# Kernel optimization log

Measured on AMD Instinct MI355X. Metric: run time of the kernel, lower is better.

The kernel has to match this reference:

```python
import jax, jax.numpy as jnp
import numpy as np

B, T, D, H = 2, 2048, 1024, 16  # batch, seq, n_embed, n_head


def setup_inputs() -> dict:
    key = jax.random.key(0)
    ks = jax.random.split(key, 5)
    scale = 1.0 / np.sqrt(D)
    return {
        "x": jax.random.normal(ks[0], (B, T, D), dtype=jnp.float32),
        "Wq": jax.random.normal(ks[1], (D, D), dtype=jnp.float32) * scale,
        "Wk": jax.random.normal(ks[2], (D, D), dtype=jnp.float32) * scale,
        "Wv": jax.random.normal(ks[3], (D, D), dtype=jnp.float32) * scale,
        "Wo": jax.random.normal(ks[4], (D, D), dtype=jnp.float32) * scale,
    }


def reference(x, Wq, Wk, Wv, Wo):
    b, t, d = x.shape
    hd = d // H  # head_dim
    # projections -> [B, H, T, hd]
    q = (x @ Wq).reshape(b, t, H, hd).transpose(0, 2, 1, 3)
    k = (x @ Wk).reshape(b, t, H, hd).transpose(0, 2, 1, 3)
    v = (x @ Wv).reshape(b, t, H, hd).transpose(0, 2, 1, 3)
    # scaled scores [B, H, T, T] with causal mask
    e = jnp.einsum("bhqd,bhkd->bhqk", q, k) * (1.0 / np.sqrt(hd))
    causal = jnp.tril(jnp.ones((t, t), dtype=bool))
    e = jnp.where(causal[None, None], e, jnp.finfo(e.dtype).min)
    alpha = jax.nn.softmax(e, axis=-1)
    # attention output -> [B, T, D]
    attn = jnp.einsum("bhqk,bhkd->bhqd", alpha, v)
    attn = attn.transpose(0, 2, 1, 3).reshape(b, t, d)
    return attn @ Wo
```

## Files before the change

### kernel.cpp

```cpp
#include <hip/hip_runtime.h>
#include <hip/hip_bf16.h>
#include <math.h>


#define Bsz  2
#define Tseq 2048
#define Dm   1024
#define NH   16
#define HD   64

typedef short bf16x8 __attribute__((ext_vector_type(8)));
typedef float floatx4 __attribute__((ext_vector_type(4)));

__device__ __forceinline__ unsigned short f2bf(float f) {
    __hip_bfloat16 h = __float2bfloat16(f);
    return *reinterpret_cast<unsigned short*>(&h);
}

__device__ __forceinline__ unsigned short f2bf_fast(float f) {
    unsigned int u = __builtin_bit_cast(unsigned int, f);
    return (unsigned short)((u + 0x8000u) >> 16);
}

__device__ __forceinline__ void lds16(unsigned short* lds, const unsigned short* g) {
    __builtin_amdgcn_global_load_lds(
        (const __attribute__((address_space(1))) void*)g,
        (__attribute__((address_space(3))) void*)lds, 16, 0, 0);
}

__global__ __launch_bounds__(256) void prep(const float* __restrict__ x,
                                            const float* __restrict__ W0,
                                            const float* __restrict__ W1,
                                            const float* __restrict__ W2,
                                            const float* __restrict__ W3,
                                            unsigned short* __restrict__ xb,
                                            unsigned short* __restrict__ T0,
                                            unsigned short* __restrict__ T1,
                                            unsigned short* __restrict__ T2,
                                            unsigned short* __restrict__ T3) {
    __shared__ float t[64][65];
    const int z = blockIdx.z;
    if (z >= 4) {
        const int bi = (z - 4) * 256 + blockIdx.y * 16 + blockIdx.x;
        const size_t i = (size_t)bi * 256 + threadIdx.x;
        const float4 v = ((const float4*)x)[i];
        ushort4 o;
        o.x = f2bf(v.x); o.y = f2bf(v.y); o.z = f2bf(v.z); o.w = f2bf(v.w);
        ((ushort4*)xb)[i] = o;
        return;
    }
    const float* W = (z == 0) ? W0 : (z == 1) ? W1 : (z == 2) ? W2 : W3;
    unsigned short* T = (z == 0) ? T0 : (z == 1) ? T1 : (z == 2) ? T2 : T3;
    const int k0 = blockIdx.y * 64, n0 = blockIdx.x * 64;
    const int row = threadIdx.x >> 6, col = threadIdx.x & 63;
#pragma unroll
    for (int p = 0; p < 16; ++p)
        t[p * 4 + row][col] = W[(size_t)(k0 + p * 4 + row) * Dm + n0 + col];
    __syncthreads();
#pragma unroll
    for (int p = 0; p < 16; ++p)
        T[(size_t)(n0 + p * 4 + row) * Dm + k0 + col] = f2bf(t[col][p * 4 + row]);
}

__device__ __forceinline__ void gemm128_mainloop(const unsigned short* __restrict__ A,
                                                 const unsigned short* __restrict__ Bt,
                                                 int K, int m0, int n0,
                                                 unsigned short* As, unsigned short* Bs,
                                                 floatx4 acc[4][4]) {
    const int tid = threadIdx.x;
    const int lane = tid & 63, wave = tid >> 6;
    const int l15 = lane & 15, quad = lane >> 4;
    const int wm = (wave >> 1) * 64, wn = (wave & 1) * 64;

    for (int k0 = 0; k0 < K; k0 += 32) {
        __syncthreads();
#pragma unroll
        for (int c = 0; c < 2; ++c) {
            const int idx = c * 256 + tid;
            const int row = idx >> 2, kc = (idx & 3) * 8;
            lds16(&As[row * 32 + kc], A + (size_t)(m0 + row) * K + k0 + kc);
            lds16(&Bs[row * 32 + kc], Bt + (size_t)(n0 + row) * K + k0 + kc);
        }
        __syncthreads();
        bf16x8 af[4], bf[4];
#pragma unroll
        for (int i = 0; i < 4; ++i)
            af[i] = *(const bf16x8*)&As[(wm + i * 16 + l15) * 32 + quad * 8];
#pragma unroll
        for (int j = 0; j < 4; ++j)
            bf[j] = *(const bf16x8*)&Bs[(wn + j * 16 + l15) * 32 + quad * 8];
#pragma unroll
        for (int i = 0; i < 4; ++i)
#pragma unroll
            for (int j = 0; j < 4; ++j)
                acc[i][j] = __builtin_amdgcn_mfma_f32_16x16x32_bf16(af[i], bf[j], acc[i][j], 0, 0, 0);
    }
}

__global__ __launch_bounds__(256) void gemm_qkv(const unsigned short* __restrict__ xb,
                                                const unsigned short* __restrict__ Wqt,
                                                const unsigned short* __restrict__ Wkt,
                                                const unsigned short* __restrict__ Wvt,
                                                unsigned short* __restrict__ Qb,
                                                unsigned short* __restrict__ Kb,
                                                unsigned short* __restrict__ VbT) {
    __shared__ unsigned short As[128 * 32];
    __shared__ unsigned short Bs[128 * 32];
    const int z = blockIdx.z;
    const unsigned short* Bt = (z == 0) ? Wqt : (z == 1) ? Wkt : Wvt;
    const float scale = (z == 0) ? (0.125f * 1.4426950408889634f) : 1.0f;
    const int m0 = blockIdx.y * 128, n0 = blockIdx.x * 128;

    floatx4 acc[4][4];
#pragma unroll
    for (int i = 0; i < 4; ++i)
#pragma unroll
        for (int j = 0; j < 4; ++j) acc[i][j] = (floatx4){0.f, 0.f, 0.f, 0.f};

    gemm128_mainloop(xb, Bt, Dm, m0, n0, As, Bs, acc);

    const int lane = threadIdx.x & 63, wave = threadIdx.x >> 6;
    const int l15 = lane & 15, quad = lane >> 4;
    const int wm = (wave >> 1) * 64, wn = (wave & 1) * 64;

    if (z == 2) {
#pragma unroll
        for (int i = 0; i < 4; ++i)
#pragma unroll
            for (int j = 0; j < 4; ++j) {
                const int col = n0 + wn + j * 16 + l15;
                const int hh = col >> 6, dd = col & 63;
                const int tok = m0 + wm + i * 16 + quad * 4;
                const int bb = tok >> 11, tl = tok & (Tseq - 1);
                ushort4 o;
                o.x = f2bf(acc[i][j][0]); o.y = f2bf(acc[i][j][1]);
                o.z = f2bf(acc[i][j][2]); o.w = f2bf(acc[i][j][3]);
                *(ushort4*)&VbT[((size_t)((bb * NH + hh) * HD + dd)) * Tseq + tl] = o;
            }
        return;
    }
    unsigned short* C = (z == 0) ? Qb : Kb;
#pragma unroll
    for (int i = 0; i < 4; ++i)
#pragma unroll
        for (int j = 0; j < 4; ++j)
#pragma unroll
            for (int r = 0; r < 4; ++r) {
                const int row = m0 + wm + i * 16 + quad * 4 + r;
                const int col = n0 + wn + j * 16 + l15;
                C[(size_t)row * Dm + col] = f2bf(acc[i][j][r] * scale);
            }
}

__global__ __launch_bounds__(256) void gemm_out(const unsigned short* __restrict__ Yb,
                                                const unsigned short* __restrict__ Wot,
                                                float* __restrict__ out) {
    __shared__ unsigned short As[64 * 32];
    __shared__ unsigned short Bs[64 * 32];
    const int m0 = blockIdx.y * 64, n0 = blockIdx.x * 64;
    const int tid = threadIdx.x;
    const int lane = tid & 63, wave = tid >> 6;
    const int l15 = lane & 15, quad = lane >> 4;
    const int wm = (wave >> 1) * 32, wn = (wave & 1) * 32;

    floatx4 acc[2][2];
#pragma unroll
    for (int i = 0; i < 2; ++i)
#pragma unroll
        for (int j = 0; j < 2; ++j) acc[i][j] = (floatx4){0.f, 0.f, 0.f, 0.f};

    const int srow = tid >> 2, kc = (tid & 3) * 8;

    for (int k0 = 0; k0 < Dm; k0 += 32) {
        __syncthreads();
        lds16(&As[srow * 32 + kc], Yb + (size_t)(m0 + srow) * Dm + k0 + kc);
        lds16(&Bs[srow * 32 + kc], Wot + (size_t)(n0 + srow) * Dm + k0 + kc);
        __syncthreads();
        bf16x8 af[2], bf[2];
#pragma unroll
        for (int i = 0; i < 2; ++i)
            af[i] = *(const bf16x8*)&As[(wm + i * 16 + l15) * 32 + quad * 8];
#pragma unroll
        for (int j = 0; j < 2; ++j)
            bf[j] = *(const bf16x8*)&Bs[(wn + j * 16 + l15) * 32 + quad * 8];
#pragma unroll
        for (int i = 0; i < 2; ++i)
#pragma unroll
            for (int j = 0; j < 2; ++j)
                acc[i][j] = __builtin_amdgcn_mfma_f32_16x16x32_bf16(af[i], bf[j], acc[i][j], 0, 0, 0);
    }

#pragma unroll
    for (int i = 0; i < 2; ++i)
#pragma unroll
        for (int j = 0; j < 2; ++j)
#pragma unroll
            for (int r = 0; r < 4; ++r) {
                const int row = m0 + wm + i * 16 + quad * 4 + r;
                const int col = n0 + wn + j * 16 + l15;
                out[(size_t)row * Dm + col] = acc[i][j][r];
            }
}

__global__ __launch_bounds__(256) void attn_mfma(const unsigned short* __restrict__ Qb,
                                                 const unsigned short* __restrict__ Kb,
                                                 const unsigned short* __restrict__ VbT,
                                                 unsigned short* __restrict__ Yb) {
    const int bh = blockIdx.x;
    const int b = bh >> 4;
    const int h = bh & 15;
    const int qt = 31 - blockIdx.y;
    const int tid = threadIdx.x;
    const int wave = tid >> 6;
    const int lane = tid & 63;
    const int l15 = lane & 15;
    const int quad = lane >> 4;

    __shared__ unsigned short Ks0[2][64][32];
    __shared__ unsigned short Ks1[2][64][32];
    __shared__ unsigned short Vt0[2][64][32];
    __shared__ unsigned short Vt1[2][64][32];
    __shared__ unsigned short Ps[4][16][72];

    const size_t tok0 = (size_t)b * Tseq;
    const int colh = h * HD;
    const unsigned short* vbase = VbT + (size_t)bh * HD * Tseq;

    const int qrow = qt * 64 + wave * 16;

    const unsigned short* qptr = Qb + (tok0 + qrow + l15) * Dm + colh + quad * 8;
    const bf16x8 qf0 = *(const bf16x8*)(qptr);
    const bf16x8 qf1 = *(const bf16x8*)(qptr + 32);

    float l_lane = 0.f;
    floatx4 o_acc[4];
#pragma unroll
    for (int t = 0; t < 4; ++t) o_acc[t] = (floatx4){0.f, 0.f, 0.f, 0.f};

    const int srow = tid >> 2;
    const int sc8 = (tid & 3) * 8;
    const int ssw = ((tid & 3) ^ ((srow >> 1) & 3)) * 8;
    const int qsw = (quad ^ ((l15 >> 1) & 3)) * 8;

    const int niter = (qt + 2) >> 1;
    for (int it = 0; it < niter; ++it) {
        const int k0 = it * 128;
        __syncthreads();
#pragma unroll
        for (int s = 0; s < 2; ++s) {
            const unsigned short* krow = Kb + (tok0 + k0 + s * 64 + srow) * Dm + colh;
            const unsigned short* vrow = vbase + (size_t)srow * Tseq + k0 + s * 64;
            lds16(&Ks0[s][srow][sc8], krow + ssw);
            lds16(&Ks1[s][srow][sc8], krow + 32 + ssw);
            lds16(&Vt0[s][srow][sc8], vrow + ssw);
            lds16(&Vt1[s][srow][sc8], vrow + 32 + ssw);
        }
        __syncthreads();

#pragma unroll
        for (int s = 0; s < 2; ++s) {
            const int k0s = k0 + s * 64;
            if (k0s > qrow + 15) continue;

            floatx4 sf[4];
#pragma unroll
            for (int t = 0; t < 4; ++t) {
                floatx4 c = (floatx4){0.f, 0.f, 0.f, 0.f};
                const bf16x8 kb0 = *(const bf16x8*)&Ks0[s][t * 16 + l15][qsw];
                const bf16x8 kb1 = *(const bf16x8*)&Ks1[s][t * 16 + l15][qsw];
                c = __builtin_amdgcn_mfma_f32_16x16x32_bf16(kb0, qf0, c, 0, 0, 0);
                c = __builtin_amdgcn_mfma_f32_16x16x32_bf16(kb1, qf1, c, 0, 0, 0);
                sf[t] = c;
            }

            if (k0s + 63 > qrow) {
                const int ql = qrow + l15;
#pragma unroll
                for (int t = 0; t < 4; ++t)
#pragma unroll
                    for (int r = 0; r < 4; ++r) {
                        const int kl = k0s + t * 16 + quad * 4 + r;
                        if (kl > ql) sf[t][r] = -1.0e30f;
                    }
            }

#pragma unroll
            for (int t = 0; t < 4; ++t) {
                float p0 = __builtin_amdgcn_exp2f(sf[t][0]);
                float p1 = __builtin_amdgcn_exp2f(sf[t][1]);
                float p2 = __builtin_amdgcn_exp2f(sf[t][2]);
                float p3 = __builtin_amdgcn_exp2f(sf[t][3]);
                l_lane += (p0 + p1) + (p2 + p3);
                ushort4 o;
                o.x = f2bf_fast(p0); o.y = f2bf_fast(p1);
                o.z = f2bf_fast(p2); o.w = f2bf_fast(p3);
                *(ushort4*)&Ps[wave][l15][t * 16 + quad * 4] = o;
            }

            const bf16x8 pa0 = *(const bf16x8*)&Ps[wave][l15][quad * 8];
            const bf16x8 pa1 = *(const bf16x8*)&Ps[wave][l15][32 + quad * 8];
#pragma unroll
            for (int t = 0; t < 4; ++t) {
                const bf16x8 vb0 = *(const bf16x8*)&Vt0[s][t * 16 + l15][qsw];
                const bf16x8 vb1 = *(const bf16x8*)&Vt1[s][t * 16 + l15][qsw];
                o_acc[t] = __builtin_amdgcn_mfma_f32_16x16x32_bf16(pa0, vb0, o_acc[t], 0, 0, 0);
                o_acc[t] = __builtin_amdgcn_mfma_f32_16x16x32_bf16(pa1, vb1, o_acc[t], 0, 0, 0);
            }
        }
    }

    l_lane += __shfl_xor(l_lane, 16);
    l_lane += __shfl_xor(l_lane, 32);
    const float inv_q = 1.0f / l_lane;
    float inv_r[4];
#pragma unroll
    for (int r = 0; r < 4; ++r)
        inv_r[r] = __shfl(inv_q, (lane & 48) | (quad * 4 + r));
#pragma unroll
    for (int t = 0; t < 4; ++t)
#pragma unroll
        for (int r = 0; r < 4; ++r) {
            const int q = qrow + quad * 4 + r;
            Yb[(tok0 + q) * Dm + colh + t * 16 + l15] = f2bf(o_acc[t][r] * inv_r[r]);
        }
}

extern "C" void kernel_launch(void* const* d_in, const int* in_sizes, int n_in,
                              void* d_out, int out_size, void* d_ws, size_t ws_size,
                              hipStream_t stream) {
    const float* x  = (const float*)d_in[0];
    const float* Wq = (const float*)d_in[1];
    const float* Wk = (const float*)d_in[2];
    const float* Wv = (const float*)d_in[3];
    const float* Wo = (const float*)d_in[4];
    float* out = (float*)d_out;

    const int M = Bsz * Tseq;
    char* ws = (char*)d_ws;
    unsigned short* xb  = (unsigned short*)(ws);
    unsigned short* Wqt = (unsigned short*)(ws + (((size_t)8)  << 20));
    unsigned short* Wkt = (unsigned short*)(ws + (((size_t)10) << 20));
    unsigned short* Wvt = (unsigned short*)(ws + (((size_t)12) << 20));
    unsigned short* Wot = (unsigned short*)(ws + (((size_t)14) << 20));
    unsigned short* Qb  = (unsigned short*)(ws + (((size_t)16) << 20));
    unsigned short* Kb  = (unsigned short*)(ws + (((size_t)24) << 20));
    unsigned short* VbT = (unsigned short*)(ws + (((size_t)32) << 20));
    unsigned short* Yb  = (unsigned short*)(ws + (((size_t)40) << 20));

    dim3 blk(256);
    hipLaunchKernelGGL(prep, dim3(16, 16, 20), blk, 0, stream,
                       x, Wq, Wk, Wv, Wo, xb, Wqt, Wkt, Wvt, Wot);

    hipLaunchKernelGGL(gemm_qkv, dim3(Dm / 128, M / 128, 3), blk, 0, stream,
                       xb, Wqt, Wkt, Wvt, Qb, Kb, VbT);

    hipLaunchKernelGGL(attn_mfma, dim3(Bsz * NH, 32), blk, 0, stream, Qb, Kb, VbT, Yb);

    hipLaunchKernelGGL(gemm_out, dim3(Dm / 64, M / 64), blk, 0, stream, Yb, Wot, out);
}
```

Before: 168.0 us.

## Double-buffer K/V tiles in attention kernel and raise MFMA wave priority

Adds a second LDS buffer for the K and V tiles, prefetched with async global-to-LDS loads. The next 128-key tile now loads while the current one is computed, with one vmcnt wait and barrier per iteration instead of two syncthreads around a blocking load. It also raises the wave priority (s_setprio) around the MFMA blocks. This doubles the LDS footprint of the attention kernel, which may lower occupancy.

```diff
diff --git a/kernel.cpp b/kernel.cpp
--- a/kernel.cpp
+++ b/kernel.cpp
@@ -216,10 +216,10 @@
     const int l15 = lane & 15;
     const int quad = lane >> 4;
 
-    __shared__ unsigned short Ks0[2][64][32];
-    __shared__ unsigned short Ks1[2][64][32];
-    __shared__ unsigned short Vt0[2][64][32];
-    __shared__ unsigned short Vt1[2][64][32];
+    __shared__ unsigned short Ks0[2][2][64][32];
+    __shared__ unsigned short Ks1[2][2][64][32];
+    __shared__ unsigned short Vt0[2][2][64][32];
+    __shared__ unsigned short Vt1[2][2][64][32];
     __shared__ unsigned short Ps[4][16][72];
 
     const size_t tok0 = (size_t)b * Tseq;
@@ -243,19 +243,41 @@
     const int qsw = (quad ^ ((l15 >> 1) & 3)) * 8;
 
     const int niter = (qt + 2) >> 1;
+
+    {
+        const unsigned short* krow0 = Kb + (tok0 + srow) * Dm + colh;
+        const unsigned short* krow1 = Kb + (tok0 + 64 + srow) * Dm + colh;
+        const unsigned short* vrow = vbase + (size_t)srow * Tseq;
+        lds16(&Ks0[0][0][srow][sc8], krow0 + ssw);
+        lds16(&Ks1[0][0][srow][sc8], krow0 + 32 + ssw);
+        lds16(&Vt0[0][0][srow][sc8], vrow + ssw);
+        lds16(&Vt1[0][0][srow][sc8], vrow + 32 + ssw);
+        lds16(&Ks0[0][1][srow][sc8], krow1 + ssw);
+        lds16(&Ks1[0][1][srow][sc8], krow1 + 32 + ssw);
+        lds16(&Vt0[0][1][srow][sc8], vrow + 64 + ssw);
+        lds16(&Vt1[0][1][srow][sc8], vrow + 64 + 32 + ssw);
+    }
+    asm volatile("s_waitcnt vmcnt(0)" ::: "memory");
+    __builtin_amdgcn_s_barrier();
+    __builtin_amdgcn_sched_barrier(0);
+
     for (int it = 0; it < niter; ++it) {
         const int k0 = it * 128;
-        __syncthreads();
-#pragma unroll
-        for (int s = 0; s < 2; ++s) {
-            const unsigned short* krow = Kb + (tok0 + k0 + s * 64 + srow) * Dm + colh;
-            const unsigned short* vrow = vbase + (size_t)srow * Tseq + k0 + s * 64;
-            lds16(&Ks0[s][srow][sc8], krow + ssw);
-            lds16(&Ks1[s][srow][sc8], krow + 32 + ssw);
-            lds16(&Vt0[s][srow][sc8], vrow + ssw);
-            lds16(&Vt1[s][srow][sc8], vrow + 32 + ssw);
+        const int bi = it & 1;
+
+        if (it + 1 < niter) {
+            const int kn = k0 + 128;
+#pragma unroll
+            for (int s = 0; s < 2; ++s) {
+                const unsigned short* krow = Kb + (tok0 + kn + s * 64 + srow) * Dm + colh;
+                const unsigned short* vrow = vbase + (size_t)srow * Tseq + kn + s * 64;
+                lds16(&Ks0[bi ^ 1][s][srow][sc8], krow + ssw);
+                lds16(&Ks1[bi ^ 1][s][srow][sc8], krow + 32 + ssw);
+                lds16(&Vt0[bi ^ 1][s][srow][sc8], vrow + ssw);
+                lds16(&Vt1[bi ^ 1][s][srow][sc8], vrow + 32 + ssw);
+            }
         }
-        __syncthreads();
+        __builtin_amdgcn_sched_barrier(0);
 
 #pragma unroll
         for (int s = 0; s < 2; ++s) {
@@ -263,15 +285,17 @@
             if (k0s > qrow + 15) continue;
 
             floatx4 sf[4];
+            __builtin_amdgcn_s_setprio(1);
 #pragma unroll
             for (int t = 0; t < 4; ++t) {
                 floatx4 c = (floatx4){0.f, 0.f, 0.f, 0.f};
-                const bf16x8 kb0 = *(const bf16x8*)&Ks0[s][t * 16 + l15][qsw];
-                const bf16x8 kb1 = *(const bf16x8*)&Ks1[s][t * 16 + l15][qsw];
+                const bf16x8 kb0 = *(const bf16x8*)&Ks0[bi][s][t * 16 + l15][qsw];
+                const bf16x8 kb1 = *(const bf16x8*)&Ks1[bi][s][t * 16 + l15][qsw];
                 c = __builtin_amdgcn_mfma_f32_16x16x32_bf16(kb0, qf0, c, 0, 0, 0);
                 c = __builtin_amdgcn_mfma_f32_16x16x32_bf16(kb1, qf1, c, 0, 0, 0);
                 sf[t] = c;
             }
+            __builtin_amdgcn_s_setprio(0);
 
             if (k0s + 63 > qrow) {
                 const int ql = qrow + l15;
@@ -299,14 +323,20 @@
 
             const bf16x8 pa0 = *(const bf16x8*)&Ps[wave][l15][quad * 8];
             const bf16x8 pa1 = *(const bf16x8*)&Ps[wave][l15][32 + quad * 8];
+            __builtin_amdgcn_s_setprio(1);
 #pragma unroll
             for (int t = 0; t < 4; ++t) {
-                const bf16x8 vb0 = *(const bf16x8*)&Vt0[s][t * 16 + l15][qsw];
-                const bf16x8 vb1 = *(const bf16x8*)&Vt1[s][t * 16 + l15][qsw];
+                const bf16x8 vb0 = *(const bf16x8*)&Vt0[bi][s][t * 16 + l15][qsw];
+                const bf16x8 vb1 = *(const bf16x8*)&Vt1[bi][s][t * 16 + l15][qsw];
                 o_acc[t] = __builtin_amdgcn_mfma_f32_16x16x32_bf16(pa0, vb0, o_acc[t], 0, 0, 0);
                 o_acc[t] = __builtin_amdgcn_mfma_f32_16x16x32_bf16(pa1, vb1, o_acc[t], 0, 0, 0);
             }
+            __builtin_amdgcn_s_setprio(0);
         }
+
+        asm volatile("s_waitcnt vmcnt(0)" ::: "memory");
+        __builtin_amdgcn_s_barrier();
+        __builtin_amdgcn_sched_barrier(0);
     }
 
     l_lane += __shfl_xor(l_lane, 16);
```

Measured after the change: 173.2 us. 3.1% more time.
